# Kernel optimization log

Hardware: AMD Instinct MI355X
Metric: run time of the kernel (lower is better)

The kernel has to match this reference:

```python
import jax, jax.numpy as jnp
import numpy as np

N_NODES = 100000
N_EDGES = 1600000
IN_C = 128
HID_C = 128
OUT_C = 64
N_GRAPHS = 64


def setup_inputs() -> dict:
    key = jax.random.key(0)
    ks = jax.random.split(key, 12)
    x = jax.random.normal(ks[0], (N_NODES, IN_C), dtype=jnp.float32)
    edge_index = jax.random.randint(ks[1], (2, N_EDGES), 0, N_NODES, dtype=jnp.int64)
    batch = jnp.sort(jax.random.randint(ks[2], (N_NODES,), 0, N_GRAPHS, dtype=jnp.int64))
    def glorot(k, fan_in, fan_out):
        s = jnp.sqrt(6.0 / (fan_in + fan_out))
        return jax.random.uniform(k, (fan_in, fan_out), jnp.float32, -s, s)
    W1 = glorot(ks[3], IN_C, HID_C);  b1 = jnp.zeros((HID_C,), jnp.float32)
    W2 = glorot(ks[4], HID_C, HID_C); b2 = jnp.zeros((HID_C,), jnp.float32)
    W3 = glorot(ks[5], HID_C, HID_C); b3 = jnp.zeros((HID_C,), jnp.float32)
    Wlin = glorot(ks[6], HID_C, OUT_C)
    blin = jnp.zeros((OUT_C,), jnp.float32)
    return {"x": x, "edge_index": edge_index, "batch": batch,
            "W1": W1, "b1": b1, "W2": W2, "b2": b2, "W3": W3, "b3": b3,
            "Wlin": Wlin, "blin": blin}


def _gcn_conv(x, W, b, src, dst, norm):
    # PyG GCNConv: h = x @ W; out[dst] += norm * h[src]; out += b
    h = x @ W
    msg = h[src] * norm[:, None]                     # [E+N, C] edge-wise gather (memory-bound)
    out = jax.ops.segment_sum(msg, dst, num_segments=N_NODES)
    return out + b


def reference(x, edge_index, batch, W1, b1, W2, b2, W3, b3, Wlin, blin):
    # add self-loops (PyG default add_self_loops=True)
    loops = jnp.arange(N_NODES, dtype=edge_index.dtype)
    src = jnp.concatenate([edge_index[0], loops])
    dst = jnp.concatenate([edge_index[1], loops])
    # symmetric normalization: deg over dst with unit edge weights
    deg = jax.ops.segment_sum(jnp.ones_like(src, dtype=x.dtype), dst, num_segments=N_NODES)
    dinv = jnp.where(deg > 0, jax.lax.rsqrt(deg), 0.0)
    norm = dinv[src] * dinv[dst]                     # [E+N]

    h = jax.nn.relu(_gcn_conv(x, W1, b1, src, dst, norm))
    h = jax.nn.relu(_gcn_conv(h, W2, b2, src, dst, norm))
    h = jax.nn.relu(_gcn_conv(h, W3, b3, src, dst, norm))

    # global mean pool over graphs
    sums = jax.ops.segment_sum(h, batch, num_segments=N_GRAPHS)
    cnts = jax.ops.segment_sum(jnp.ones((N_NODES,), h.dtype), batch, num_segments=N_GRAPHS)
    pooled = sums / jnp.clip(cnts, 1.0)[:, None]     # [G, HID_C]
    return pooled @ Wlin + blin                      # [G, OUT_C]
```

## Files before the change

### kernel.cpp

```cpp
#include <hip/hip_runtime.h>
#include <stdint.h>

#define C_HID 128
#define NGRAPH 64
#define COUT 64
#define POOL_S 64
#define NBLK 256
#define BKT 256
#define NBUK_MAX 512
#define SCAN_CH 4096

typedef short bf16x8 __attribute__((ext_vector_type(8)));
typedef float f32x4 __attribute__((ext_vector_type(4)));
typedef float f32x2 __attribute__((ext_vector_type(2)));

__device__ __forceinline__ unsigned short f2bf(float f){
  unsigned int u = __builtin_bit_cast(unsigned int, f);
  u = u + 0x7FFFu + ((u >> 16) & 1u);
  return (unsigned short)(u >> 16);
}
__device__ __forceinline__ float bflo(unsigned int u){
  return __builtin_bit_cast(float, u << 16);
}
__device__ __forceinline__ float bfhi(unsigned int u){
  return __builtin_bit_cast(float, u & 0xFFFF0000u);
}
__device__ __forceinline__ int clampi(int v, int lo, int hi){
  return v < lo ? lo : (v > hi ? hi : v);
}

__global__ void k_zero(float* __restrict__ out, int n){
  int i = blockIdx.x*blockDim.x + threadIdx.x;
  if (i < n) out[i] = 0.f;
}

__global__ __launch_bounds__(256) void k_cnt(const int* __restrict__ dst,
                                             int* __restrict__ cntg,
                                             int E, int N, int NBUK, int chunk){
  __shared__ int cnt[NBUK_MAX];
  int blk = blockIdx.x, t = threadIdx.x;
  for (int b = t; b < NBUK; b += 256) cnt[b] = 0;
  __syncthreads();
  int e0 = blk*chunk, e1 = min(E, e0 + chunk);
  for (int e = e0 + t; e < e1; e += 256)
    atomicAdd(&cnt[clampi(dst[e], 0, N-1) >> 8], 1);
  __syncthreads();
  for (int b = t; b < NBUK; b += 256)
    cntg[b*NBLK + blk] = cnt[b];
}

__global__ __launch_bounds__(256) void k_scanA(const int* __restrict__ cnt,
                                               int* __restrict__ bsum, int n){
  __shared__ int red[256];
  int blk = blockIdx.x, t = threadIdx.x;
  int base = blk*SCAN_CH + t*16;
  int s = 0;
  #pragma unroll
  for (int j = 0; j < 16; ++j){ int i = base + j; s += (i < n) ? cnt[i] : 0; }
  red[t] = s; __syncthreads();
  for (int off = 128; off > 0; off >>= 1){
    if (t < off) red[t] += red[t + off];
    __syncthreads();
  }
  if (t == 0) bsum[blk] = red[0];
}

__global__ __launch_bounds__(256) void k_scanB(const int* __restrict__ bsum,
                                               int* __restrict__ bbase,
                                               int* __restrict__ bases, int nb, int n){
  __shared__ int buf[256];
  int t = threadIdx.x;
  int v = (t < nb) ? bsum[t] : 0;
  buf[t] = v; __syncthreads();
  for (int off = 1; off < 256; off <<= 1){
    int add = (t >= off) ? buf[t-off] : 0;
    __syncthreads();
    buf[t] += add;
    __syncthreads();
  }
  if (t < nb) bbase[t] = buf[t] - v;
  if (t == nb-1) bases[n] = buf[t];
}

__global__ __launch_bounds__(256) void k_scanC(const int* __restrict__ cnt,
                                               const int* __restrict__ bbase,
                                               int* __restrict__ bases, int n){
  __shared__ int buf[256];
  int blk = blockIdx.x, t = threadIdx.x;
  int base = blk*SCAN_CH + t*16;
  int loc[16]; int s = 0;
  #pragma unroll
  for (int j = 0; j < 16; ++j){ int i = base + j; loc[j] = (i < n) ? cnt[i] : 0; s += loc[j]; }
  buf[t] = s; __syncthreads();
  for (int off = 1; off < 256; off <<= 1){
    int add = (t >= off) ? buf[t-off] : 0;
    __syncthreads();
    buf[t] += add;
    __syncthreads();
  }
  int run = bbase[blk] + buf[t] - s;
  #pragma unroll
  for (int j = 0; j < 16; ++j){
    int i = base + j;
    if (i < n) bases[i] = run;
    run += loc[j];
  }
}

__global__ __launch_bounds__(256) void k_scat(const int* __restrict__ src,
                                              const int* __restrict__ dst,
                                              const int* __restrict__ bases,
                                              unsigned int* __restrict__ rec,
                                              int E, int N, int NBUK, int chunk){
  __shared__ int cur[NBUK_MAX];
  int blk = blockIdx.x, t = threadIdx.x;
  for (int b = t; b < NBUK; b += 256) cur[b] = bases[b*NBLK + blk];
  __syncthreads();
  int e0 = blk*chunk, e1 = min(E, e0 + chunk);
  for (int e = e0 + t; e < e1; e += 256){
    int d = clampi(dst[e], 0, N-1);
    int s = clampi(src[e], 0, N-1);
    int p = atomicAdd(&cur[d >> 8], 1);
    rec[p] = (unsigned int)s | ((unsigned int)(d & 255) << 24);
  }
}

__global__ __launch_bounds__(256) void k_csr(const unsigned int* __restrict__ rec,
                                             const int* __restrict__ bases,
                                             int* __restrict__ offs, float* __restrict__ dinv,
                                             int* __restrict__ meta, int E, int N, int NBUK){
  __shared__ int cnt[BKT], loff[BKT], cur[BKT];
  int b = blockIdx.x, t = threadIdx.x;
  cnt[t] = 0;
  __syncthreads();
  int r0 = bases[b*NBLK];
  int r1 = (b+1 < NBUK) ? bases[(b+1)*NBLK] : E;
  for (int i = r0 + t; i < r1; i += 256)
    atomicAdd(&cnt[rec[i] >> 24], 1);
  __syncthreads();
  loff[t] = cnt[t];
  __syncthreads();
  for (int off = 1; off < BKT; off <<= 1){
    int add = (t >= off) ? loff[t - off] : 0;
    __syncthreads();
    loff[t] += add;
    __syncthreads();
  }
  int excl = loff[t] - cnt[t];
  cur[t] = r0 + excl;
  int node = b*BKT + t;
  if (node < N){
    offs[node] = r0 + excl;
    dinv[node] = rsqrtf((float)(cnt[t] + 1));
  }
  if (b == NBUK-1 && t == 0) offs[N] = E;
  __syncthreads();
  for (int i = r0 + t; i < r1; i += 256){
    unsigned int r = rec[i];
    int p = atomicAdd(&cur[r >> 24], 1);
    meta[p] = (int)(r & 0x00FFFFFFu);
  }
}

__global__ void k_xcast(const float2* __restrict__ x, const float* __restrict__ dinv,
                        unsigned short* __restrict__ y, unsigned short* __restrict__ y2, int N){
  int i = blockIdx.x*256 + threadIdx.x;
  int tot = N*64;
  if (i < tot){
    float2 v = x[i];
    float dn = dinv[i >> 6] * 64.f;
    int p = __builtin_amdgcn_cvt_pk_fp8_f32(v.x*dn, v.y*dn, 0, false);
    y[i] = (unsigned short)(p & 0xFFFF);
  } else if (i < tot + 64){
    y[i] = 0;
    y2[i] = 0;
  }
}

__global__ void k_prep(const float* __restrict__ W1, const float* __restrict__ W2,
                       const float* __restrict__ W3, unsigned short* __restrict__ Wt){
  int idx = blockIdx.x*256 + threadIdx.x;
  int w = idx >> 14;
  int r = idx & 16383;
  int n = r & 127, k = r >> 7;
  const float* W = (w == 0) ? W1 : (w == 1) ? W2 : W3;
  Wt[(size_t)w*16384 + (size_t)n*128 + k] = f2bf(W[k*128 + n]);
}

__global__ __launch_bounds__(256) void k_spmm(const unsigned short* __restrict__ y,
                       const int* __restrict__ offs,
                       const float* __restrict__ dinv,
                       const int* __restrict__ meta,
                       unsigned int* __restrict__ agg, int N){
  int wv   = __builtin_amdgcn_readfirstlane(threadIdx.x >> 6);
  int lane = threadIdx.x & 63;
  int node = blockIdx.x*4 + wv;
  if (node >= N) return;
  int g = lane >> 4;
  int c = lane & 15;

  int e0 = offs[node], e1 = offs[node+1];
  int cnt = e1 - e0;
  int mv = (lane < cnt) ? meta[e0 + lane] : N;

  const uint2* yrow = (const uint2*)y;

  f32x2 acc[4];
  #pragma unroll
  for (int k = 0; k < 4; ++k) acc[k] = (f32x2){0.f, 0.f};

  int nslot = cnt + 1;
  int ninstr = (nslot + 3) >> 2;
  if (ninstr > 8) ninstr = 8;

  uint2 u[8];
  #pragma unroll
  for (int k = 0; k < 8; ++k){
    if (k < ninstr){
      int slot = k*4 + g;
      int idx  = slot - 1;
      int idxc = idx < 0 ? 0 : idx;
      int sj = __shfl(mv, idxc, 64);
      if (slot == 0) sj = node;
      u[k] = yrow[(size_t)sj*16 + c];
    }
  }
  __builtin_amdgcn_sched_barrier(0);
  #pragma unroll
  for (int k = 0; k < 8; ++k){
    if (k < ninstr){
      f32x2 f;
      f = __builtin_amdgcn_cvt_pk_f32_fp8((int)u[k].x, false); acc[0] += f;
      f = __builtin_amdgcn_cvt_pk_f32_fp8((int)u[k].x, true);  acc[1] += f;
      f = __builtin_amdgcn_cvt_pk_f32_fp8((int)u[k].y, false); acc[2] += f;
      f = __builtin_amdgcn_cvt_pk_f32_fp8((int)u[k].y, true);  acc[3] += f;
    }
  }
  for (int base = 32; base < nslot; base += 4){
    int idx = base + g - 1;
    int sj = (idx < cnt) ? meta[e0 + idx] : N;
    uint2 t = yrow[(size_t)sj*16 + c];
    f32x2 f;
    f = __builtin_amdgcn_cvt_pk_f32_fp8((int)t.x, false); acc[0] += f;
    f = __builtin_amdgcn_cvt_pk_f32_fp8((int)t.x, true);  acc[1] += f;
    f = __builtin_amdgcn_cvt_pk_f32_fp8((int)t.y, false); acc[2] += f;
    f = __builtin_amdgcn_cvt_pk_f32_fp8((int)t.y, true);  acc[3] += f;
  }
  #pragma unroll
  for (int k = 0; k < 4; ++k){
    acc[k].x += __shfl_xor(acc[k].x, 16, 64);
    acc[k].y += __shfl_xor(acc[k].y, 16, 64);
    acc[k].x += __shfl_xor(acc[k].x, 32, 64);
    acc[k].y += __shfl_xor(acc[k].y, 32, 64);
  }
  float dn = dinv[node] * 0.015625f;
  if (g == 0){
    uint4 w;
    w.x = (unsigned int)f2bf(acc[0].x*dn) | ((unsigned int)f2bf(acc[0].y*dn) << 16);
    w.y = (unsigned int)f2bf(acc[1].x*dn) | ((unsigned int)f2bf(acc[1].y*dn) << 16);
    w.z = (unsigned int)f2bf(acc[2].x*dn) | ((unsigned int)f2bf(acc[2].y*dn) << 16);
    w.w = (unsigned int)f2bf(acc[3].x*dn) | ((unsigned int)f2bf(acc[3].y*dn) << 16);
    *(uint4*)(agg + (size_t)node*64 + c*4) = w;
  }
}

#define GEMM_BLOCKS 512
template<bool FP8OUT>
__global__ __launch_bounds__(256) void k_gemm(const unsigned short* __restrict__ A,
                                              const unsigned short* __restrict__ Wt,
                                              const float* __restrict__ bias,
                                              const float* __restrict__ scale,
                                              void* __restrict__ outv, int M){
  __shared__ unsigned short wt[128*136];
  {
    const uint4* wsrc = (const uint4*)Wt;
    for (int i = threadIdx.x; i < 4096; i += 256){
      uint4 v = wsrc[i];
      int n = i >> 4, kblk = i & 15;
      *(uint4*)&wt[n*136 + kblk*8] = v;
    }
  }
  __syncthreads();

  int wv = threadIdx.x >> 6, lane = threadIdx.x & 63;
  int q = lane >> 4, ln = lane & 15;
  int tiles = (M + 63) >> 6;

  for (int tile = blockIdx.x; tile < tiles; tile += GEMM_BLOCKS){
    int m0 = tile*64 + wv*16;
    int arow = m0 + ln;
    bool arow_ok = (arow < M);
    int arow_s = arow_ok ? arow : 0;

    f32x4 zero = {0.f, 0.f, 0.f, 0.f};
    f32x4 acc[8];
    #pragma unroll
    for (int t = 0; t < 8; ++t) acc[t] = zero;

    #pragma unroll
    for (int kk = 0; kk < 4; ++kk){
      bf16x8 a;
      if (arow_ok){
        __builtin_memcpy(&a, A + (size_t)arow_s*128 + kk*32 + q*8, 16);
      } else {
        a = (bf16x8){0,0,0,0,0,0,0,0};
      }
      #pragma unroll
      for (int t = 0; t < 8; ++t){
        bf16x8 b;
        __builtin_memcpy(&b, &wt[(t*16 + ln)*136 + kk*32 + q*8], 16);
        acc[t] = __builtin_amdgcn_mfma_f32_16x16x32_bf16(a, b, acc[t], 0, 0, 0);
      }
    }
    float sc[4];
    #pragma unroll
    for (int r = 0; r < 4; ++r){
      int row = m0 + q*4 + r;
      sc[r] = (FP8OUT && row < M) ? scale[row] * 64.f : 1.0f;
    }
    #pragma unroll
    for (int t = 0; t < 8; ++t){
      float bv = bias[t*16 + ln];
      #pragma unroll
      for (int r = 0; r < 4; ++r){
        int row = m0 + q*4 + r;
        if (row < M){
          float v = acc[t][r] + bv;
          v = v > 0.f ? v : 0.f;
          if (FP8OUT){
            v *= sc[r];
            int p = __builtin_amdgcn_cvt_pk_fp8_f32(v, v, 0, false);
            ((unsigned char*)outv)[(size_t)row*128 + t*16 + ln] = (unsigned char)(p & 0xFF);
          } else {
            ((unsigned short*)outv)[(size_t)row*128 + t*16 + ln] = f2bf(v);
          }
        }
      }
    }
  }
}

__device__ __forceinline__ int lower_bound_i(const int* arr, int n, int val){
  int lo = 0, hi = n;
  while (lo < hi){ int mid = (lo + hi) >> 1; if (arr[mid] < val) lo = mid + 1; else hi = mid; }
  return lo;
}

__global__ void k_pool(const unsigned int* __restrict__ x, const int* __restrict__ batch,
                       float* __restrict__ partial, int N){
  int g = blockIdx.x / POOL_S, s = blockIdx.x % POOL_S;
  int h = threadIdx.x >> 6;
  int lane = threadIdx.x & 63;
  int rs = clampi(lower_bound_i(batch, N, g), 0, N);
  int re = clampi(lower_bound_i(batch, N, g + 1), rs, N);
  int len = re - rs;
  int a = rs + (int)(((long long)len * s) / POOL_S);
  int b = rs + (int)(((long long)len * (s + 1)) / POOL_S);
  float ax = 0.f, ay = 0.f;
  for (int i = a + h; i < b; i += 2){
    unsigned int u = x[(size_t)i*64 + lane];
    ax += bflo(u);
    ay += bfhi(u);
  }
  float* p = partial + ((size_t)(g*POOL_S + s)*2 + h)*C_HID;
  p[2*lane]   = ax;
  p[2*lane+1] = ay;
}

__global__ void k_final(const float* __restrict__ partial, const int* __restrict__ batch,
                        const float* __restrict__ Wl, const float* __restrict__ bl,
                        float* __restrict__ out, int N){
  __shared__ float sums[C_HID];
  int g = blockIdx.x;
  int t = threadIdx.x;
  float acc = 0.f;
  const float* p = partial + (size_t)g*POOL_S*2*C_HID;
  for (int j = 0; j < POOL_S*2; ++j)
    acc += p[j*C_HID + t];
  sums[t] = acc;
  __syncthreads();
  if (t < COUT){
    int rs = clampi(lower_bound_i(batch, N, g), 0, N);
    int re = clampi(lower_bound_i(batch, N, g + 1), rs, N);
    float inv = 1.0f / fmaxf((float)(re - rs), 1.0f);
    float o = 0.f;
    for (int k = 0; k < 128; ++k)
      o += sums[k] * Wl[k*COUT + t];
    out[g*COUT + t] = o * inv + bl[t];
  }
}

extern "C" void kernel_launch(void* const* d_in, const int* in_sizes, int n_in,
                              void* d_out, int out_size, void* d_ws, size_t ws_size,
                              hipStream_t stream){
  const float* x0 = (const float*)d_in[0];
  const int* ei   = (const int*)d_in[1];
  const int* batch= (const int*)d_in[2];
  const float* W1 = (const float*)d_in[3];
  const float* b1 = (const float*)d_in[4];
  const float* W2 = (const float*)d_in[5];
  const float* b2 = (const float*)d_in[6];
  const float* W3 = (const float*)d_in[7];
  const float* b3 = (const float*)d_in[8];
  const float* Wl = (const float*)d_in[9];
  const float* bl = (const float*)d_in[10];
  float* out = (float*)d_out;

  int E = in_sizes[1] / 2;
  int N = in_sizes[2];
  const int* src = ei;
  const int* dst = ei + E;
  int NBUK = (N + BKT - 1) / BKT;
  int chunk = (E + NBLK - 1) / NBLK;
  int ncnt = NBUK * NBLK;
  int nsb  = (ncnt + SCAN_CH - 1) / SCAN_CH;

  size_t off_acc = 0;
  auto carve = [&](size_t bytes)->size_t{
    size_t r = off_acc; off_acc += (bytes + 255) & ~(size_t)255; return r;
  };
  size_t o_cnt   = carve((size_t)ncnt*4);
  size_t o_bases = carve((size_t)(ncnt+1)*4);
  size_t o_bsum  = carve(256*4);
  size_t o_bbase = carve(256*4);
  size_t o_offs  = carve((size_t)(N+1)*4);
  size_t o_dinv  = carve((size_t)N*4);
  size_t o_meta  = carve((size_t)E*4);
  size_t o_rec   = carve((size_t)E*4);
  size_t o_yA    = carve((size_t)(N+1)*C_HID);
  size_t o_yB    = carve((size_t)(N+1)*C_HID);
  size_t o_aggb  = carve((size_t)N*C_HID*2);
  size_t o_wt    = carve((size_t)3*128*128*2);
  size_t need = off_acc;

  size_t hbuf_avail = o_aggb - o_meta;
  bool alias_ok = hbuf_avail >= (size_t)N*C_HID*2;
  alias_ok = alias_ok &&
             ((size_t)(N+1)*C_HID >= (size_t)NGRAPH*POOL_S*2*C_HID*4);

  if (ws_size < need || NBUK > NBUK_MAX || nsb > 256 || !alias_ok){
    k_zero<<<(out_size+255)/256, 256, 0, stream>>>(out, out_size);
    return;
  }

  char* base = (char*)d_ws;
  int* cntg  = (int*)(base + o_cnt);
  int* bases = (int*)(base + o_bases);
  int* bsum  = (int*)(base + o_bsum);
  int* bbase = (int*)(base + o_bbase);
  int* offs  = (int*)(base + o_offs);
  float* dinv= (float*)(base + o_dinv);
  int* meta  = (int*)(base + o_meta);
  unsigned int* rec   = (unsigned int*)(base + o_rec);
  unsigned short* yA  = (unsigned short*)(base + o_yA);
  unsigned short* yB  = (unsigned short*)(base + o_yB);
  unsigned int* aggb  = (unsigned int*)(base + o_aggb);
  unsigned short* wt  = (unsigned short*)(base + o_wt);
  unsigned short* hbuf= (unsigned short*)(base + o_meta);
  float* part         = (float*)(base + o_yB);

  k_cnt  <<<NBLK, 256, 0, stream>>>(dst, cntg, E, N, NBUK, chunk);
  k_scanA<<<nsb, 256, 0, stream>>>(cntg, bsum, ncnt);
  k_scanB<<<1, 256, 0, stream>>>(bsum, bbase, bases, nsb, ncnt);
  k_scanC<<<nsb, 256, 0, stream>>>(cntg, bbase, bases, ncnt);
  k_scat <<<NBLK, 256, 0, stream>>>(src, dst, bases, rec, E, N, NBUK, chunk);
  k_csr  <<<NBUK, BKT, 0, stream>>>(rec, bases, offs, dinv, meta, E, N, NBUK);

  k_xcast<<<(N*64 + 64 + 255)/256, 256, 0, stream>>>((const float2*)x0, dinv, yA, yB, N);
  k_prep <<<192, 256, 0, stream>>>(W1, W2, W3, wt);

  int spmm_grid = (N + 3) / 4;

  k_spmm<<<spmm_grid, 256, 0, stream>>>(yA, offs, dinv, meta, aggb, N);
  k_gemm<true ><<<GEMM_BLOCKS, 256, 0, stream>>>((const unsigned short*)aggb, wt,           b1, dinv, (void*)yB, N);
  k_spmm<<<spmm_grid, 256, 0, stream>>>(yB, offs, dinv, meta, aggb, N);
  k_gemm<true ><<<GEMM_BLOCKS, 256, 0, stream>>>((const unsigned short*)aggb, wt + 16384,   b2, dinv, (void*)yA, N);
  k_spmm<<<spmm_grid, 256, 0, stream>>>(yA, offs, dinv, meta, aggb, N);
  k_gemm<false><<<GEMM_BLOCKS, 256, 0, stream>>>((const unsigned short*)aggb, wt + 2*16384, b3, dinv, (void*)hbuf, N);

  k_pool <<<NGRAPH*POOL_S, 128, 0, stream>>>((const unsigned int*)hbuf, batch, part, N);
  k_final<<<NGRAPH, 128, 0, stream>>>(part, batch, Wl, bl, out, N);
}
```

Before: 387.8 us.

## Process four nodes per wavefront in SpMM with 16-lane groups per node

Reworks the SpMM so each wavefront handles four destination nodes, one per 16-lane group, instead of one node spread over four groups. Neighbor indices are broadcast inside each group with ds_swizzle, and the cross-group shuffle reduction goes away. Gathers are issued in fixed batches of eight, gated by the largest degree among the four nodes. This trades shorter reduction work for load imbalance between nodes of different degree and some padded gathers to row N.

```diff
diff --git a/kernel.cpp b/kernel.cpp
--- a/kernel.cpp
+++ b/kernel.cpp
@@ -194,73 +194,97 @@
                        unsigned int* __restrict__ agg, int N){
   int wv   = __builtin_amdgcn_readfirstlane(threadIdx.x >> 6);
   int lane = threadIdx.x & 63;
-  int node = blockIdx.x*4 + wv;
-  if (node >= N) return;
-  int g = lane >> 4;
-  int c = lane & 15;
-
-  int e0 = offs[node], e1 = offs[node+1];
-  int cnt = e1 - e0;
-  int mv = (lane < cnt) ? meta[e0 + lane] : N;
+  int g = lane >> 4, c = lane & 15;
+  int node0 = blockIdx.x*16 + wv*4;
+  if (node0 >= N) return;
+
+  int eA = offs[node0];
+  int eB = offs[min(node0+1, N)];
+  int eC = offs[min(node0+2, N)];
+  int eD = offs[min(node0+3, N)];
+  int eE = offs[min(node0+4, N)];
+  int c0 = eB-eA, c1 = eC-eB, c2 = eD-eC, c3 = eE-eD;
+  int maxc = max(max(c0,c1), max(c2,c3));
+
+  int e0l  = (g==0) ? eA : (g==1) ? eB : (g==2) ? eC : eD;
+  int cntl = (g==0) ? c0 : (g==1) ? c1 : (g==2) ? c2 : c3;
+  int nodeg = node0 + g;
+  bool nok = nodeg < N;
+  int nself = nok ? nodeg : N;
 
   const uint2* yrow = (const uint2*)y;
 
+  int mv0 = (c < cntl)      ? meta[e0l + c]      : N;
+  int mv1 = (c + 16 < cntl) ? meta[e0l + c + 16] : N;
+  uint2 us = yrow[(size_t)nself*16 + c];
+  float dl = dinv[nok ? nodeg : 0];
+
   f32x2 acc[4];
-  #pragma unroll
-  for (int k = 0; k < 4; ++k) acc[k] = (f32x2){0.f, 0.f};
-
-  int nslot = cnt + 1;
-  int ninstr = (nslot + 3) >> 2;
-  if (ninstr > 8) ninstr = 8;
+  { f32x2 f;
+    f = __builtin_amdgcn_cvt_pk_f32_fp8((int)us.x, false); acc[0] = f;
+    f = __builtin_amdgcn_cvt_pk_f32_fp8((int)us.x, true);  acc[1] = f;
+    f = __builtin_amdgcn_cvt_pk_f32_fp8((int)us.y, false); acc[2] = f;
+    f = __builtin_amdgcn_cvt_pk_f32_fp8((int)us.y, true);  acc[3] = f; }
 
   uint2 u[8];
-  #pragma unroll
-  for (int k = 0; k < 8; ++k){
-    if (k < ninstr){
-      int slot = k*4 + g;
-      int idx  = slot - 1;
-      int idxc = idx < 0 ? 0 : idx;
-      int sj = __shfl(mv, idxc, 64);
-      if (slot == 0) sj = node;
-      u[k] = yrow[(size_t)sj*16 + c];
-    }
-  }
-  __builtin_amdgcn_sched_barrier(0);
-  #pragma unroll
-  for (int k = 0; k < 8; ++k){
-    if (k < ninstr){
-      f32x2 f;
-      f = __builtin_amdgcn_cvt_pk_f32_fp8((int)u[k].x, false); acc[0] += f;
-      f = __builtin_amdgcn_cvt_pk_f32_fp8((int)u[k].x, true);  acc[1] += f;
-      f = __builtin_amdgcn_cvt_pk_f32_fp8((int)u[k].y, false); acc[2] += f;
-      f = __builtin_amdgcn_cvt_pk_f32_fp8((int)u[k].y, true);  acc[3] += f;
-    }
-  }
-  for (int base = 32; base < nslot; base += 4){
-    int idx = base + g - 1;
-    int sj = (idx < cnt) ? meta[e0 + idx] : N;
-    uint2 t = yrow[(size_t)sj*16 + c];
+#define SWZ0(J) __builtin_amdgcn_ds_swizzle(mv0, (0x10 | (((J)&15)<<5)))
+#define SWZ1(J) __builtin_amdgcn_ds_swizzle(mv1, (0x10 | (((J)&15)<<5)))
+#define GA(K, SM) u[K] = yrow[(size_t)(unsigned)(SM)*16 + c]
+#define CONV8() do{ _Pragma("unroll") \
+  for (int k2 = 0; k2 < 8; ++k2){ \
+    f32x2 f; \
+    f = __builtin_amdgcn_cvt_pk_f32_fp8((int)u[k2].x, false); acc[0] += f; \
+    f = __builtin_amdgcn_cvt_pk_f32_fp8((int)u[k2].x, true);  acc[1] += f; \
+    f = __builtin_amdgcn_cvt_pk_f32_fp8((int)u[k2].y, false); acc[2] += f; \
+    f = __builtin_amdgcn_cvt_pk_f32_fp8((int)u[k2].y, true);  acc[3] += f; } }while(0)
+
+  if (0 < maxc){
+    GA(0,SWZ0(0)); GA(1,SWZ0(1)); GA(2,SWZ0(2)); GA(3,SWZ0(3));
+    GA(4,SWZ0(4)); GA(5,SWZ0(5)); GA(6,SWZ0(6)); GA(7,SWZ0(7));
+    __builtin_amdgcn_sched_barrier(0);
+    CONV8();
+  }
+  if (8 < maxc){
+    GA(0,SWZ0(8)); GA(1,SWZ0(9)); GA(2,SWZ0(10)); GA(3,SWZ0(11));
+    GA(4,SWZ0(12)); GA(5,SWZ0(13)); GA(6,SWZ0(14)); GA(7,SWZ0(15));
+    __builtin_amdgcn_sched_barrier(0);
+    CONV8();
+  }
+  if (16 < maxc){
+    GA(0,SWZ1(16)); GA(1,SWZ1(17)); GA(2,SWZ1(18)); GA(3,SWZ1(19));
+    GA(4,SWZ1(20)); GA(5,SWZ1(21)); GA(6,SWZ1(22)); GA(7,SWZ1(23));
+    __builtin_amdgcn_sched_barrier(0);
+    CONV8();
+  }
+  if (24 < maxc){
+    GA(0,SWZ1(24)); GA(1,SWZ1(25)); GA(2,SWZ1(26)); GA(3,SWZ1(27));
+    GA(4,SWZ1(28)); GA(5,SWZ1(29)); GA(6,SWZ1(30)); GA(7,SWZ1(31));
+    __builtin_amdgcn_sched_barrier(0);
+    CONV8();
+  }
+#undef SWZ0
+#undef SWZ1
+#undef GA
+#undef CONV8
+
+  for (int j = 32; j < maxc; ++j){
+    int sm = (j < cntl) ? meta[e0l + j] : N;
+    uint2 t = yrow[(size_t)(unsigned)sm*16 + c];
     f32x2 f;
     f = __builtin_amdgcn_cvt_pk_f32_fp8((int)t.x, false); acc[0] += f;
     f = __builtin_amdgcn_cvt_pk_f32_fp8((int)t.x, true);  acc[1] += f;
     f = __builtin_amdgcn_cvt_pk_f32_fp8((int)t.y, false); acc[2] += f;
     f = __builtin_amdgcn_cvt_pk_f32_fp8((int)t.y, true);  acc[3] += f;
   }
-  #pragma unroll
-  for (int k = 0; k < 4; ++k){
-    acc[k].x += __shfl_xor(acc[k].x, 16, 64);
-    acc[k].y += __shfl_xor(acc[k].y, 16, 64);
-    acc[k].x += __shfl_xor(acc[k].x, 32, 64);
-    acc[k].y += __shfl_xor(acc[k].y, 32, 64);
-  }
-  float dn = dinv[node] * 0.015625f;
-  if (g == 0){
+
+  float dn = dl * 0.015625f;
+  if (nok){
     uint4 w;
     w.x = (unsigned int)f2bf(acc[0].x*dn) | ((unsigned int)f2bf(acc[0].y*dn) << 16);
     w.y = (unsigned int)f2bf(acc[1].x*dn) | ((unsigned int)f2bf(acc[1].y*dn) << 16);
     w.z = (unsigned int)f2bf(acc[2].x*dn) | ((unsigned int)f2bf(acc[2].y*dn) << 16);
     w.w = (unsigned int)f2bf(acc[3].x*dn) | ((unsigned int)f2bf(acc[3].y*dn) << 16);
-    *(uint4*)(agg + (size_t)node*64 + c*4) = w;
+    *(uint4*)(agg + (size_t)nodeg*64 + c*4) = w;
   }
 }
 
@@ -469,7 +493,7 @@
   k_xcast<<<(N*64 + 64 + 255)/256, 256, 0, stream>>>((const float2*)x0, dinv, yA, yB, N);
   k_prep <<<192, 256, 0, stream>>>(W1, W2, W3, wt);
 
-  int spmm_grid = (N + 3) / 4;
+  int spmm_grid = (N + 15) / 16;
 
   k_spmm<<<spmm_grid, 256, 0, stream>>>(yA, offs, dinv, meta, aggb, N);
   k_gemm<true ><<<GEMM_BLOCKS, 256, 0, stream>>>((const unsigned short*)aggb, wt,           b1, dinv, (void*)yB, N);
```

After: 338.0 us. 12.9% less time.
